# Kernel tuning notes

Measured on AMD Instinct MI355X. Metric: run time of the kernel, lower is better.

The kernel has to match this reference:

```python
import jax, jax.numpy as jnp
import numpy as np

B = 4        # pair batch
V = 2        # num_views
C = 256      # channels
NH = 4       # num_heads
H = 128
W = 128
G = 8        # GroupNorm groups
EPS = 1e-5


def setup_inputs() -> dict:
    key = jax.random.key(0)
    ks = jax.random.split(key, 5)
    x = jax.random.normal(ks[0], (B * V, C, H, W), jnp.float32)
    gn_gamma = jnp.ones((C,), jnp.float32)
    gn_beta = jnp.zeros((C,), jnp.float32)
    w_qkv = jax.random.normal(ks[1], (3 * C, C), jnp.float32) * 0.02
    b_qkv = jax.random.normal(ks[2], (3 * C,), jnp.float32) * 0.02
    w_proj = jax.random.normal(ks[3], (C, C), jnp.float32) * 0.02
    b_proj = jax.random.normal(ks[4], (C,), jnp.float32) * 0.02
    return {"x": x, "gn_gamma": gn_gamma, "gn_beta": gn_beta,
            "w_qkv": w_qkv, "b_qkv": b_qkv, "w_proj": w_proj, "b_proj": b_proj}


def reference(x, gn_gamma, gn_beta, w_qkv, b_qkv, w_proj, b_proj):
    bv, c, h, w = x.shape
    v, nh = V, NH
    hd = c // nh
    b = bv // v
    scale = hd ** -0.5

    # GroupNorm(8, c): normalize over (c/G, h, w) per group, biased variance
    xg = x.reshape(bv, G, c // G, h, w)
    mean = xg.mean(axis=(2, 3, 4), keepdims=True)
    var = xg.var(axis=(2, 3, 4), keepdims=True)
    xn = ((xg - mean) * jax.lax.rsqrt(var + EPS)).reshape(bv, c, h, w)
    xn = xn * gn_gamma[:, None, None] + gn_beta[:, None, None]

    # 1x1 conv qkv: (bv, 3c, h, w)
    qkv = jnp.einsum('oc,bchw->bohw', w_qkv, xn) + b_qkv[:, None, None]

    # '(b v) (three nh hd) h w -> three b nh (h w) v hd'
    qkv = qkv.reshape(b, v, 3, nh, hd, h * w).transpose(2, 0, 3, 5, 1, 4)
    q, k, val = qkv[0], qkv[1], qkv[2]  # each (b, nh, hw, v, hd)

    # tiny VxV attention per pixel
    attn = jax.nn.softmax(jnp.einsum('bnpvd,bnpud->bnpvu', q, k) * scale, axis=-1)
    out = jnp.einsum('bnpvu,bnpud->bnpvd', attn, val)  # (b, nh, hw, v, hd)

    # 'b nh (h w) v hd -> (b v) (nh hd) h w'
    out = out.transpose(0, 3, 1, 4, 2).reshape(bv, c, h, w)

    # proj 1x1 conv + residual
    out = jnp.einsum('oc,bchw->bohw', w_proj, out) + b_proj[:, None, None]
    return x + out
```

## Files before the change

### kernel.cpp

```cpp
#include <hip/hip_runtime.h>
#include <stdint.h>

#define HW 16384
#define CCH 256
#define NROWS 131072
#define GROUP_ELEMS 524288
#define BK 64
#define LDSP 72
#define PADC 198

typedef __attribute__((ext_vector_type(8))) short bfrag8;
typedef __attribute__((ext_vector_type(8))) unsigned short us8;
typedef __attribute__((ext_vector_type(4))) float facc4;

static __device__ __forceinline__ unsigned short f2b(float f) {
  union { float f; unsigned int u; } x; x.f = f;
  unsigned int r = x.u + 0x7FFFu + ((x.u >> 16) & 1u);
  return (unsigned short)(r >> 16);
}
static __device__ __forceinline__ float b2f(unsigned short h) {
  union { float f; unsigned int u; } x; x.u = ((unsigned int)h) << 16;
  return x.f;
}

__global__ void k_red(const float* __restrict__ x, float* __restrict__ red) {
  int gg = blockIdx.x >> 3, sp = blockIdx.x & 7;
  const float4* p = (const float4*)(x + (size_t)gg * GROUP_ELEMS + (size_t)sp * 65536);
  float s = 0.f, ss = 0.f;
  for (int i = 0; i < 64; ++i) {
    float4 v = p[i * 256 + threadIdx.x];
    s  += v.x + v.y + v.z + v.w;
    ss += v.x*v.x + v.y*v.y + v.z*v.z + v.w*v.w;
  }
  for (int off = 32; off; off >>= 1) { s += __shfl_xor(s, off); ss += __shfl_xor(ss, off); }
  __shared__ float ls[4], lss[4];
  int w = threadIdx.x >> 6;
  if ((threadIdx.x & 63) == 0) { ls[w] = s; lss[w] = ss; }
  __syncthreads();
  if (threadIdx.x == 0) {
    float S = ls[0]+ls[1]+ls[2]+ls[3], SS = lss[0]+lss[1]+lss[2]+lss[3];
    atomicAdd(&red[gg*2], S); atomicAdd(&red[gg*2+1], SS);
  }
}

__global__ void k_fin(const float* __restrict__ red, float* __restrict__ stats) {
  int g = threadIdx.x;
  float s = red[g*2], ss = red[g*2+1];
  float mean = s / (float)GROUP_ELEMS;
  float var = ss / (float)GROUP_ELEMS - mean*mean;
  stats[g*2] = mean;
  stats[g*2+1] = rsqrtf(var + 1e-5f);
}

__global__ void k_cast(const float* __restrict__ wq, const float* __restrict__ wp,
                       unsigned short* __restrict__ wqb, unsigned short* __restrict__ wpb) {
  int i = blockIdx.x * 256 + threadIdx.x;
  if (i < 768*256) {
    int op = i >> 8, k = i & 255;
    int h = op / 192, cl = op % 192;
    int part = cl >> 6, d = cl & 63;
    int o = part*256 + h*64 + d;
    wqb[i] = f2b(wq[o*256 + k]);
  } else {
    int j = i - 768*256;
    wpb[j] = f2b(wp[j]);
  }
}

__global__ void k_norm_t(const float* __restrict__ x, const float* __restrict__ stats,
                         const float* __restrict__ gamma, const float* __restrict__ beta,
                         unsigned short* __restrict__ xnt) {
  __shared__ float tile[64][65];
  int bx = blockIdx.x;
  int bv = bx >> 10;
  int rem = bx & 1023;
  int p0 = (rem >> 2) * 64, c0 = (rem & 3) * 64;
  int pair = bv >> 1, v = bv & 1;
  int t = threadIdx.x;
  int p_off = t & 63, c4 = t >> 6;
  const float* xsrc = x + (size_t)bv * CCH * HW;
  for (int cc = 0; cc < 16; ++cc) {
    int c_loc = c4 * 16 + cc;
    int c = c0 + c_loc;
    float val = xsrc[(size_t)c * HW + p0 + p_off];
    int g = bv * 8 + (c >> 5);
    float xn = (val - stats[g*2]) * stats[g*2+1] * gamma[c] + beta[c];
    tile[p_off][c_loc] = xn;
  }
  __syncthreads();
  for (int it = 0; it < 8; ++it) {
    int u = it * 256 + t;
    int p = u >> 5, c2 = u & 31;
    unsigned int pk = (unsigned int)f2b(tile[p][c2*2]) | ((unsigned int)f2b(tile[p][c2*2+1]) << 16);
    size_t row = (size_t)pair * 32768 + (size_t)(p0 + p) * 2 + v;
    *(unsigned int*)(xnt + row * 256 + c0 + c2*2) = pk;
  }
}

__global__ __launch_bounds__(256, 2) void k_qkv_attn(
    const unsigned short* __restrict__ A,
    const unsigned short* __restrict__ B,
    const float* __restrict__ bq,
    unsigned short* __restrict__ attn_out) {
  __shared__ __align__(16) unsigned short smem[128 * PADC];
  __shared__ float sW[256];
  unsigned short* As = smem;
  unsigned short* Bs = smem + 128 * LDSP;
  int h = blockIdx.x;
  int row0 = blockIdx.y * 128;
  int t = threadIdx.x;
  int w = t >> 6, lane = t & 63;
  int wm = w & 1, wn = w >> 1;
  int lm = lane & 15, q = lane >> 4;
  facc4 acc[4][6] = {};
  const unsigned short* Bh = B + (size_t)h * 192 * 256;
  for (int kc = 0; kc < 4; ++kc) {
    for (int i = 0; i < 4; ++i) {
      int flat = i * 256 + t;
      int r = flat >> 3, g = flat & 7;
      *(us8*)(&As[r*LDSP + g*8]) = *(const us8*)(A + (size_t)(row0 + r)*256 + kc*BK + g*8);
    }
    for (int i = 0; i < 6; ++i) {
      int flat = i * 256 + t;
      int r = flat >> 3, g = flat & 7;
      *(us8*)(&Bs[r*LDSP + g*8]) = *(const us8*)(Bh + (size_t)r*256 + kc*BK + g*8);
    }
    __syncthreads();
    for (int ks = 0; ks < 2; ++ks) {
      bfrag8 a[4], b[6];
      for (int i = 0; i < 4; ++i) a[i] = *(const bfrag8*)(&As[(wm*64 + i*16 + lm)*LDSP + ks*32 + q*8]);
      for (int j = 0; j < 6; ++j) b[j] = *(const bfrag8*)(&Bs[(wn*96 + j*16 + lm)*LDSP + ks*32 + q*8]);
      for (int i = 0; i < 4; ++i)
        for (int j = 0; j < 6; ++j)
          acc[i][j] = __builtin_amdgcn_mfma_f32_16x16x32_bf16(a[i], b[j], acc[i][j], 0, 0, 0);
    }
    __syncthreads();
  }
  unsigned short* sT = smem;
  for (int j = 0; j < 6; ++j) {
    int cl = wn*96 + j*16 + lm;
    int part = cl >> 6, d = cl & 63;
    float bi = bq[part*256 + h*64 + d];
    for (int i = 0; i < 4; ++i) {
      int rl = wm*64 + i*16 + q*4;
      for (int r = 0; r < 4; ++r)
        sT[(rl + r)*PADC + cl] = f2b(acc[i][j][r] + bi);
    }
  }
  __syncthreads();
  {
    int px = t >> 2, s = t & 3;
    int qv = s >> 1, kv = s & 1;
    const unsigned short* qrow = sT + (2*px + qv)*PADC;
    const unsigned short* krow = sT + (2*px + kv)*PADC + 64;
    float dot = 0.f;
    for (int d = 0; d < 64; ++d) dot += b2f(qrow[d]) * b2f(krow[d]);
    dot *= 0.125f;
    float other = __shfl_xor(dot, 1);
    float m = fmaxf(dot, other);
    float e = __expf(dot - m), eo = __expf(other - m);
    sW[px*4 + s] = e / (e + eo);
  }
  __syncthreads();
  int gp0 = blockIdx.y * 64;
  for (int it = 0; it < 32; ++it) {
    int u = it * 256 + t;
    int d = u & 63, vv = (u >> 6) & 1, px = u >> 7;
    float v0 = b2f(sT[(2*px)*PADC + 128 + d]);
    float v1 = b2f(sT[(2*px + 1)*PADC + 128 + d]);
    float o = sW[px*4 + vv*2] * v0 + sW[px*4 + vv*2 + 1] * v1;
    int g = gp0 + px;
    int pair = g >> 14, p = g & 16383;
    attn_out[((size_t)(pair*2 + vv) * 16384 + p) * 256 + h*64 + d] = f2b(o);
  }
}

__global__ __launch_bounds__(256, 2) void k_gemm_proj(
    const unsigned short* __restrict__ A,
    const unsigned short* __restrict__ B,
    const float* __restrict__ bias,
    const float* __restrict__ x,
    float* __restrict__ out) {
  __shared__ unsigned short As[128][LDSP];
  __shared__ unsigned short Bs[128][LDSP];
  int col0 = blockIdx.x * 128;
  int row0 = blockIdx.y * 128;
  int t = threadIdx.x;
  int w = t >> 6, lane = t & 63;
  int wm = w & 1, wn = w >> 1;
  int lm = lane & 15, q = lane >> 4;
  facc4 acc[4][4] = {};
  for (int kc = 0; kc < 4; ++kc) {
    for (int i = 0; i < 4; ++i) {
      int flat = i * 256 + t;
      int r = flat >> 3, g = flat & 7;
      *(us8*)(&As[r][g*8]) = *(const us8*)(A + (size_t)(row0 + r)*256 + kc*BK + g*8);
      *(us8*)(&Bs[r][g*8]) = *(const us8*)(B + (size_t)(col0 + r)*256 + kc*BK + g*8);
    }
    __syncthreads();
    for (int ks = 0; ks < 2; ++ks) {
      bfrag8 a[4], b[4];
      for (int i = 0; i < 4; ++i) a[i] = *(const bfrag8*)(&As[wm*64 + i*16 + lm][ks*32 + q*8]);
      for (int j = 0; j < 4; ++j) b[j] = *(const bfrag8*)(&Bs[wn*64 + j*16 + lm][ks*32 + q*8]);
      for (int i = 0; i < 4; ++i)
        for (int j = 0; j < 4; ++j)
          acc[i][j] = __builtin_amdgcn_mfma_f32_16x16x32_bf16(a[i], b[j], acc[i][j], 0, 0, 0);
    }
    __syncthreads();
  }
  for (int i = 0; i < 4; ++i) {
    for (int r = 0; r < 4; ++r) {
      int o = row0 + wm*64 + i*16 + q*4 + r;
      float bi = bias[o];
      for (int j = 0; j < 4; ++j) {
        int n = col0 + wn*64 + j*16 + lm;
        int bv = n >> 14, p = n & 16383;
        size_t gidx = ((size_t)bv * 256 + o) * 16384 + p;
        out[gidx] = acc[i][j][r] + bi + x[gidx];
      }
    }
  }
}

extern "C" void kernel_launch(void* const* d_in, const int* in_sizes, int n_in,
                              void* d_out, int out_size, void* d_ws, size_t ws_size,
                              hipStream_t stream) {
  const float* x     = (const float*)d_in[0];
  const float* gamma = (const float*)d_in[1];
  const float* beta  = (const float*)d_in[2];
  const float* wq    = (const float*)d_in[3];
  const float* bq    = (const float*)d_in[4];
  const float* wp    = (const float*)d_in[5];
  const float* bp    = (const float*)d_in[6];
  float* out = (float*)d_out;

  char* ws = (char*)d_ws;
  float* red   = (float*)ws;
  float* stats = (float*)(ws + 512);
  unsigned short* wqb = (unsigned short*)(ws + 1024);
  unsigned short* wpb = (unsigned short*)(ws + 1024 + 393216);
  size_t off = 1024 + 393216 + 131072;
  unsigned short* xnt = (unsigned short*)(ws + off); off += (size_t)NROWS * 256 * 2;
  unsigned short* att = (unsigned short*)(ws + off);

  hipMemsetAsync(red, 0, 1024, stream);
  k_cast<<<1024, 256, 0, stream>>>(wq, wp, wqb, wpb);
  k_red<<<512, 256, 0, stream>>>(x, red);
  k_fin<<<1, 64, 0, stream>>>(red, stats);
  k_norm_t<<<8192, 256, 0, stream>>>(x, stats, gamma, beta, xnt);
  k_qkv_attn<<<dim3(4, 1024), 256, 0, stream>>>(xnt, wqb, bq, att);
  k_gemm_proj<<<dim3(1024, 2), 256, 0, stream>>>(wpb, att, bp, x, out);
}
```

Before: 439.5 us.

## Compute QKV and 2-view attention in registers without LDS staging

Rewrites the fused QKV+attention kernel so each wave computes a 64-row by 192-column tile straight from global memory, with the GEMM transposed (weights as the A operand). Bias is folded into the accumulator init. The per-pixel q·k dot products, softmax and value mixing run on the MFMA accumulators using lane shuffles instead of LDS round trips and block barriers. This drops the LDS tiles and syncthreads. In exchange it uses 192 accumulator floats per thread, which pressures registers and occupancy, and it loads operands without shared reuse across waves.

```diff
diff --git a/kernel.cpp b/kernel.cpp
--- a/kernel.cpp
+++ b/kernel.cpp
@@ -7,7 +7,6 @@
 #define GROUP_ELEMS 524288
 #define BK 64
 #define LDSP 72
-#define PADC 198
 
 typedef __attribute__((ext_vector_type(8))) short bfrag8;
 typedef __attribute__((ext_vector_type(8))) unsigned short us8;
@@ -102,76 +101,75 @@
     const unsigned short* __restrict__ B,
     const float* __restrict__ bq,
     unsigned short* __restrict__ attn_out) {
-  __shared__ __align__(16) unsigned short smem[128 * PADC];
-  __shared__ float sW[256];
-  unsigned short* As = smem;
-  unsigned short* Bs = smem + 128 * LDSP;
-  int h = blockIdx.x;
-  int row0 = blockIdx.y * 128;
-  int t = threadIdx.x;
-  int w = t >> 6, lane = t & 63;
-  int wm = w & 1, wn = w >> 1;
-  int lm = lane & 15, q = lane >> 4;
-  facc4 acc[4][6] = {};
+  int h = blockIdx.y;
+  int w = threadIdx.x >> 6, lane = threadIdx.x & 63;
+  int r0 = blockIdx.x * 256 + w * 64;
+  int lm = lane & 15, q4 = lane >> 4;
   const unsigned short* Bh = B + (size_t)h * 192 * 256;
-  for (int kc = 0; kc < 4; ++kc) {
-    for (int i = 0; i < 4; ++i) {
-      int flat = i * 256 + t;
-      int r = flat >> 3, g = flat & 7;
-      *(us8*)(&As[r*LDSP + g*8]) = *(const us8*)(A + (size_t)(row0 + r)*256 + kc*BK + g*8);
-    }
-    for (int i = 0; i < 6; ++i) {
-      int flat = i * 256 + t;
-      int r = flat >> 3, g = flat & 7;
-      *(us8*)(&Bs[r*LDSP + g*8]) = *(const us8*)(Bh + (size_t)r*256 + kc*BK + g*8);
-    }
-    __syncthreads();
-    for (int ks = 0; ks < 2; ++ks) {
-      bfrag8 a[4], b[6];
-      for (int i = 0; i < 4; ++i) a[i] = *(const bfrag8*)(&As[(wm*64 + i*16 + lm)*LDSP + ks*32 + q*8]);
-      for (int j = 0; j < 6; ++j) b[j] = *(const bfrag8*)(&Bs[(wn*96 + j*16 + lm)*LDSP + ks*32 + q*8]);
+
+  facc4 acc[4][12];
+  #pragma unroll
+  for (int j = 0; j < 12; ++j) {
+    facc4 bb = *(const facc4*)(bq + (j >> 2)*256 + h*64 + (j & 3)*16 + q4*4);
+    #pragma unroll
+    for (int i = 0; i < 4; ++i) acc[i][j] = bb;
+  }
+
+  #pragma unroll
+  for (int kc = 0; kc < 8; ++kc) {
+    bfrag8 a[4];
+    #pragma unroll
+    for (int i = 0; i < 4; ++i)
+      a[i] = *(const bfrag8*)(A + (size_t)(r0 + i*16 + lm)*256 + kc*32 + q4*8);
+    #pragma unroll
+    for (int j = 0; j < 12; ++j) {
+      bfrag8 wf = *(const bfrag8*)(Bh + (size_t)(j*16 + lm)*256 + kc*32 + q4*8);
+      #pragma unroll
       for (int i = 0; i < 4; ++i)
-        for (int j = 0; j < 6; ++j)
-          acc[i][j] = __builtin_amdgcn_mfma_f32_16x16x32_bf16(a[i], b[j], acc[i][j], 0, 0, 0);
-    }
-    __syncthreads();
-  }
-  unsigned short* sT = smem;
-  for (int j = 0; j < 6; ++j) {
-    int cl = wn*96 + j*16 + lm;
-    int part = cl >> 6, d = cl & 63;
-    float bi = bq[part*256 + h*64 + d];
-    for (int i = 0; i < 4; ++i) {
-      int rl = wm*64 + i*16 + q*4;
-      for (int r = 0; r < 4; ++r)
-        sT[(rl + r)*PADC + cl] = f2b(acc[i][j][r] + bi);
-    }
-  }
-  __syncthreads();
-  {
-    int px = t >> 2, s = t & 3;
-    int qv = s >> 1, kv = s & 1;
-    const unsigned short* qrow = sT + (2*px + qv)*PADC;
-    const unsigned short* krow = sT + (2*px + kv)*PADC + 64;
-    float dot = 0.f;
-    for (int d = 0; d < 64; ++d) dot += b2f(qrow[d]) * b2f(krow[d]);
-    dot *= 0.125f;
-    float other = __shfl_xor(dot, 1);
-    float m = fmaxf(dot, other);
-    float e = __expf(dot - m), eo = __expf(other - m);
-    sW[px*4 + s] = e / (e + eo);
-  }
-  __syncthreads();
-  int gp0 = blockIdx.y * 64;
-  for (int it = 0; it < 32; ++it) {
-    int u = it * 256 + t;
-    int d = u & 63, vv = (u >> 6) & 1, px = u >> 7;
-    float v0 = b2f(sT[(2*px)*PADC + 128 + d]);
-    float v1 = b2f(sT[(2*px + 1)*PADC + 128 + d]);
-    float o = sW[px*4 + vv*2] * v0 + sW[px*4 + vv*2 + 1] * v1;
-    int g = gp0 + px;
-    int pair = g >> 14, p = g & 16383;
-    attn_out[((size_t)(pair*2 + vv) * 16384 + p) * 256 + h*64 + d] = f2b(o);
+        acc[i][j] = __builtin_amdgcn_mfma_f32_16x16x32_bf16(wf, a[i], acc[i][j], 0, 0, 0);
+    }
+  }
+
+  #pragma unroll
+  for (int i = 0; i < 4; ++i) {
+    float s_same = 0.f, s_cross = 0.f;
+    #pragma unroll
+    for (int jj = 0; jj < 4; ++jj) {
+      #pragma unroll
+      for (int r = 0; r < 4; ++r) {
+        float qv = acc[i][jj][r];
+        float kv = acc[i][4 + jj][r];
+        float kx = __shfl_xor(kv, 1);
+        s_same  += qv * kv;
+        s_cross += qv * kx;
+      }
+    }
+    s_same  += __shfl_xor(s_same, 16);  s_same  += __shfl_xor(s_same, 32);
+    s_cross += __shfl_xor(s_cross, 16); s_cross += __shfl_xor(s_cross, 32);
+    float s0 = s_same * 0.125f, s1 = s_cross * 0.125f;
+    float m = fmaxf(s0, s1);
+    float e0 = __expf(s0 - m), e1 = __expf(s1 - m);
+    float inv = 1.f / (e0 + e1);
+    float w_self = e0 * inv, w_cross = e1 * inv;
+
+    int rglob = r0 + i*16 + lm;
+    int pair = rglob >> 15, rem = rglob & 32767;
+    int p = rem >> 1, v = rem & 1;
+    unsigned short* dst = attn_out + ((size_t)((pair*2 + v)*16384 + p))*256 + h*64 + q4*4;
+    #pragma unroll
+    for (int jj = 0; jj < 4; ++jj) {
+      float o[4];
+      #pragma unroll
+      for (int r = 0; r < 4; ++r) {
+        float vv = acc[i][8 + jj][r];
+        float vx = __shfl_xor(vv, 1);
+        o[r] = w_self * vv + w_cross * vx;
+      }
+      uint2 pk;
+      pk.x = (unsigned int)f2b(o[0]) | ((unsigned int)f2b(o[1]) << 16);
+      pk.y = (unsigned int)f2b(o[2]) | ((unsigned int)f2b(o[3]) << 16);
+      *(uint2*)(dst + jj*16) = pk;
+    }
   }
 }
 
@@ -248,6 +246,6 @@
   k_red<<<512, 256, 0, stream>>>(x, red);
   k_fin<<<1, 64, 0, stream>>>(red, stats);
   k_norm_t<<<8192, 256, 0, stream>>>(x, stats, gamma, beta, xnt);
-  k_qkv_attn<<<dim3(4, 1024), 256, 0, stream>>>(xnt, wqb, bq, att);
+  k_qkv_attn<<<dim3(512, 4), 256, 0, stream>>>(xnt, wqb, bq, att);
   k_gemm_proj<<<dim3(1024, 2), 256, 0, stream>>>(wpb, att, bp, x, out);
 }
```

Measured after the change: 645.1 us. +46.8%, slower.
